# Optimization experiments

Hardware: AMD Instinct MI355X
Metric: run time of the kernel (lower is better)

## Reference

```python
import jax, jax.numpy as jnp
import numpy as np

N_NODES = 20000
N_EDGES = 320000
BERT_H = 768
GIN_H = 256
N_LAYERS = 3
EPS = 0.0  # gin_epsilon


def setup_inputs() -> dict:
    key = jax.random.key(0)
    ks = jax.random.split(key, 12)
    node_embed = jax.random.normal(ks[0], (N_NODES, BERT_H), dtype=jnp.float32)
    edge_weight = jax.random.uniform(ks[1], (N_EDGES,), dtype=jnp.float32)
    src = jax.random.randint(ks[2], (N_EDGES,), 0, N_NODES, dtype=jnp.int32)
    dst = jax.random.randint(ks[3], (N_EDGES,), 0, N_NODES, dtype=jnp.int32)
    s = 0.02
    W0 = jax.random.normal(ks[4], (BERT_H, GIN_H), dtype=jnp.float32) * s
    b0 = jnp.zeros((GIN_H,), dtype=jnp.float32)
    W1 = jax.random.normal(ks[5], (GIN_H, GIN_H), dtype=jnp.float32) * s
    b1 = jnp.zeros((GIN_H,), dtype=jnp.float32)
    W2 = jax.random.normal(ks[6], (GIN_H, GIN_H), dtype=jnp.float32) * s
    b2 = jnp.zeros((GIN_H,), dtype=jnp.float32)
    Wr = jax.random.normal(ks[7], (N_LAYERS * GIN_H, GIN_H), dtype=jnp.float32) * s
    br = jnp.zeros((GIN_H,), dtype=jnp.float32)
    return {"node_embed": node_embed, "edge_weight": edge_weight,
            "W0": W0, "b0": b0, "W1": W1, "b1": b1, "W2": W2, "b2": b2,
            "Wr": Wr, "br": br, "src": src, "dst": dst}


def _gin_layer(h, edge_weight, src, dst, W, b):
    # edge-weighted sum aggregation: agg_i = sum_{(j->i)} w_ji * h_j
    msgs = h[src] * edge_weight[:, None]          # [E, d]
    agg = jax.ops.segment_sum(msgs, dst, num_segments=N_NODES)  # [N, d]
    rst = (1.0 + EPS) * h + agg
    return jax.nn.relu(rst @ W + b)


def reference(node_embed, edge_weight, W0, b0, W1, b1, W2, b2, Wr, br, src, dst):
    params = [(W0, b0), (W1, b1), (W2, b2)]
    h = node_embed
    outs = []
    for (W, b) in params:
        h = _gin_layer(h, edge_weight, src, dst, W, b)
        outs.append(h)
    cat = jnp.concatenate(outs, axis=-1)          # [N, n_layers*gin_h]
    return jax.nn.relu(cat) @ Wr + br             # [N, gin_h]
```

## Files before the change

### kernel.cpp

```cpp
#include <hip/hip_runtime.h>

#define NN 20000
#define NE 320000
#define BH 768
#define GH 256

typedef __attribute__((ext_vector_type(8))) short short8;
typedef __attribute__((ext_vector_type(4))) float f32x4;

__device__ __forceinline__ ushort f2bf(float x) {
    union { float f; unsigned u; } v; v.f = x;
    unsigned r = (v.u + 0x7FFFu + ((v.u >> 16) & 1u)) >> 16;
    return (ushort)r;
}
__device__ __forceinline__ float bf2f(ushort h) {
    union { unsigned u; float f; } v; v.u = ((unsigned)h) << 16;
    return v.f;
}

__device__ __forceinline__ void gload_lds16(const void* g, void* l) {
    __builtin_amdgcn_global_load_lds(
        (const __attribute__((address_space(1))) void*)g,
        (__attribute__((address_space(3))) void*)l, 16, 0, 0);
}


__global__ void k_count(const int* __restrict__ dst, int* __restrict__ cnt, int E) {
    int i = blockIdx.x * blockDim.x + threadIdx.x;
    if (i < E) atomicAdd(&cnt[dst[i]], 1);
}

__global__ __launch_bounds__(1024)
void k_scan(const int* __restrict__ cnt, int* __restrict__ off,
            int* __restrict__ fill, int n) {
    __shared__ int sbuf[1024];
    const int tid  = threadIdx.x;
    const int base = tid * 20;
    int local[20];
    int s = 0;
    #pragma unroll
    for (int i = 0; i < 20; ++i) {
        const int idx = base + i;
        int v = (idx < n) ? cnt[idx] : 0;
        local[i] = s;
        s += v;
    }
    sbuf[tid] = s;
    __syncthreads();
    int sum = s;
    for (int ofs = 1; ofs < 1024; ofs <<= 1) {
        int other = (tid >= ofs) ? sbuf[tid - ofs] : 0;
        __syncthreads();
        sum += other;
        sbuf[tid] = sum;
        __syncthreads();
    }
    const int excl = sum - s;
    #pragma unroll
    for (int i = 0; i < 20; ++i) {
        const int idx = base + i;
        if (idx < n) { const int v = excl + local[i]; off[idx] = v; fill[idx] = v; }
    }
    if (tid == 1023) off[n] = sum;
}

__global__ void k_scatter(const int* __restrict__ src, const int* __restrict__ dst,
                          const float* __restrict__ w, int* __restrict__ fill,
                          int* __restrict__ csr_src, float* __restrict__ csr_w, int E) {
    int i = blockIdx.x * blockDim.x + threadIdx.x;
    if (i < E) {
        int d = dst[i];
        int p = atomicAdd(&fill[d], 1);
        csr_src[p] = src[i];
        csr_w[p]  = w[i];
    }
}


__global__ void k_split(const float* __restrict__ x, ushort* __restrict__ hi,
                        ushort* __restrict__ lo, int n4) {
    int i = blockIdx.x * blockDim.x + threadIdx.x;
    if (i >= n4) return;
    float4 v = ((const float4*)x)[i];
    ushort4 h, l;
    h.x = f2bf(v.x); l.x = f2bf(v.x - bf2f(h.x));
    h.y = f2bf(v.y); l.y = f2bf(v.y - bf2f(h.y));
    h.z = f2bf(v.z); l.z = f2bf(v.z - bf2f(h.z));
    h.w = f2bf(v.w); l.w = f2bf(v.w - bf2f(h.w));
    ((ushort4*)hi)[i] = h;
    ((ushort4*)lo)[i] = l;
}

__global__ void k_splitw(const float* __restrict__ W, ushort* __restrict__ hi,
                         ushort* __restrict__ lo, int K, int N) {
    int id = blockIdx.x * blockDim.x + threadIdx.x;
    if (id >= K * N) return;
    int n = id / K, k = id % K;
    float v = W[(size_t)k * N + n];
    ushort h = f2bf(v);
    hi[id] = h;
    lo[id] = f2bf(v - bf2f(h));
}


__global__ __launch_bounds__(256)
void k_gemm_mfma(const ushort* __restrict__ Ah, const ushort* __restrict__ Al,
                 int lda, int K,
                 const ushort* __restrict__ Bh, const ushort* __restrict__ Bl,
                 const float* __restrict__ bias,
                 float* __restrict__ C, int M) {
    __shared__ ushort As_h[64 * 32];
    __shared__ ushort As_l[64 * 32];
    __shared__ ushort Bs_h[128 * 32];
    __shared__ ushort Bs_l[128 * 32];

    const int t    = threadIdx.x;
    const int lane = t & 63;
    const int m0   = blockIdx.y * 64;
    const int n0   = blockIdx.x * 128;

    const int ra = t >> 2;
    const int sa = (t & 3) ^ ((ra >> 1) & 3);
    int rga = m0 + ra; if (rga > M - 1) rga = M - 1;
    const size_t aofs = (size_t)rga * lda + (size_t)(sa * 8);
    char* a_dst_h = (char*)As_h + ((t >> 6) << 10);
    char* a_dst_l = (char*)As_l + ((t >> 6) << 10);

    const int cb1 = t + 256;
    const int rb0 = t >> 2,   rb1 = cb1 >> 2;
    const int sb0 = (t & 3)   ^ ((rb0 >> 1) & 3);
    const int sb1 = (cb1 & 3) ^ ((rb1 >> 1) & 3);
    const size_t bofs0 = (size_t)(n0 + rb0) * K + (size_t)(sb0 * 8);
    const size_t bofs1 = (size_t)(n0 + rb1) * K + (size_t)(sb1 * 8);
    char* b_dst_h0 = (char*)Bs_h + ((t >> 6) << 10);
    char* b_dst_h1 = (char*)Bs_h + ((cb1 >> 6) << 10);
    char* b_dst_l0 = (char*)Bs_l + ((t >> 6) << 10);
    char* b_dst_l1 = (char*)Bs_l + ((cb1 >> 6) << 10);

    const int wm = (t >> 6) & 1;
    const int wn = t >> 7;

    f32x4 zero = (f32x4)0.0f;
    f32x4 acc[2][4];
    #pragma unroll
    for (int i = 0; i < 2; ++i)
        #pragma unroll
        for (int j = 0; j < 4; ++j) acc[i][j] = zero;

    const int fr  = lane & 15;
    const int fsl = lane >> 4;

    for (int k0 = 0; k0 < K; k0 += 32) {
        __syncthreads();
        gload_lds16(Ah + aofs + k0, a_dst_h);
        gload_lds16(Al + aofs + k0, a_dst_l);
        gload_lds16(Bh + bofs0 + k0, b_dst_h0);
        gload_lds16(Bh + bofs1 + k0, b_dst_h1);
        gload_lds16(Bl + bofs0 + k0, b_dst_l0);
        gload_lds16(Bl + bofs1 + k0, b_dst_l1);
        __syncthreads();

        short8 ah[2], al2[2], bh[4], bl[4];
        #pragma unroll
        for (int i = 0; i < 2; ++i) {
            const int r = wm * 32 + i * 16 + fr;
            const int s = fsl ^ ((r >> 1) & 3);
            ah[i]  = *(const short8*)(As_h + r * 32 + s * 8);
            al2[i] = *(const short8*)(As_l + r * 32 + s * 8);
        }
        #pragma unroll
        for (int j = 0; j < 4; ++j) {
            const int r = wn * 64 + j * 16 + fr;
            const int s = fsl ^ ((r >> 1) & 3);
            bh[j] = *(const short8*)(Bs_h + r * 32 + s * 8);
            bl[j] = *(const short8*)(Bs_l + r * 32 + s * 8);
        }
        #pragma unroll
        for (int i = 0; i < 2; ++i)
            #pragma unroll
            for (int j = 0; j < 4; ++j) {
                acc[i][j] = __builtin_amdgcn_mfma_f32_16x16x32_bf16(ah[i],  bh[j], acc[i][j], 0, 0, 0);
                acc[i][j] = __builtin_amdgcn_mfma_f32_16x16x32_bf16(ah[i],  bl[j], acc[i][j], 0, 0, 0);
                acc[i][j] = __builtin_amdgcn_mfma_f32_16x16x32_bf16(al2[i], bh[j], acc[i][j], 0, 0, 0);
            }
    }

    #pragma unroll
    for (int i = 0; i < 2; ++i) {
        #pragma unroll
        for (int j = 0; j < 4; ++j) {
            const int col = n0 + wn * 64 + j * 16 + fr;
            const int r0  = m0 + wm * 32 + i * 16 + ((lane >> 4) << 2);
            const float ba = bias ? bias[col] : 0.0f;
            #pragma unroll
            for (int q = 0; q < 4; ++q) {
                const int r = r0 + q;
                if (r < M) C[(size_t)r * 256 + col] = acc[i][j][q] + ba;
            }
        }
    }
}


__global__ __launch_bounds__(256)
void k_aggregate(const float* __restrict__ y,
                 const int* __restrict__ off,
                 const int* __restrict__ csr_src,
                 const float* __restrict__ csr_w,
                 const float* __restrict__ bias,
                 ushort* __restrict__ cat_h,
                 ushort* __restrict__ cat_l,
                 int n) {
    const int wave = blockIdx.x * (blockDim.x >> 6) + (threadIdx.x >> 6);
    const int lane = threadIdx.x & 63;
    if (wave >= n) return;
    const int c = lane * 4;

    float4 self = *(const float4*)(y + (size_t)wave * GH + c);
    float4 b    = *(const float4*)(bias + c);

    float4 a0 = make_float4(0.f, 0.f, 0.f, 0.f);
    float4 a1 = a0, a2 = a0, a3 = a0;
    const int e0 = off[wave], e1 = off[wave + 1];
    int e = e0;
    for (; e + 4 <= e1; e += 4) {
        const int   s0 = csr_src[e],     s1 = csr_src[e + 1];
        const int   s2 = csr_src[e + 2], s3 = csr_src[e + 3];
        const float w0 = csr_w[e],       w1 = csr_w[e + 1];
        const float w2 = csr_w[e + 2],   w3 = csr_w[e + 3];
        float4 v0 = *(const float4*)(y + (size_t)s0 * GH + c);
        float4 v1 = *(const float4*)(y + (size_t)s1 * GH + c);
        float4 v2 = *(const float4*)(y + (size_t)s2 * GH + c);
        float4 v3 = *(const float4*)(y + (size_t)s3 * GH + c);
        a0.x = fmaf(w0, v0.x, a0.x); a0.y = fmaf(w0, v0.y, a0.y);
        a0.z = fmaf(w0, v0.z, a0.z); a0.w = fmaf(w0, v0.w, a0.w);
        a1.x = fmaf(w1, v1.x, a1.x); a1.y = fmaf(w1, v1.y, a1.y);
        a1.z = fmaf(w1, v1.z, a1.z); a1.w = fmaf(w1, v1.w, a1.w);
        a2.x = fmaf(w2, v2.x, a2.x); a2.y = fmaf(w2, v2.y, a2.y);
        a2.z = fmaf(w2, v2.z, a2.z); a2.w = fmaf(w2, v2.w, a2.w);
        a3.x = fmaf(w3, v3.x, a3.x); a3.y = fmaf(w3, v3.y, a3.y);
        a3.z = fmaf(w3, v3.z, a3.z); a3.w = fmaf(w3, v3.w, a3.w);
    }
    for (; e < e1; ++e) {
        const int   s = csr_src[e];
        const float w = csr_w[e];
        float4 v = *(const float4*)(y + (size_t)s * GH + c);
        a0.x = fmaf(w, v.x, a0.x); a0.y = fmaf(w, v.y, a0.y);
        a0.z = fmaf(w, v.z, a0.z); a0.w = fmaf(w, v.w, a0.w);
    }
    float4 r;
    r.x = fmaxf(self.x + ((a0.x + a1.x) + (a2.x + a3.x)) + b.x, 0.f);
    r.y = fmaxf(self.y + ((a0.y + a1.y) + (a2.y + a3.y)) + b.y, 0.f);
    r.z = fmaxf(self.z + ((a0.z + a1.z) + (a2.z + a3.z)) + b.z, 0.f);
    r.w = fmaxf(self.w + ((a0.w + a1.w) + (a2.w + a3.w)) + b.w, 0.f);
    ushort4 h, l;
    h.x = f2bf(r.x); l.x = f2bf(r.x - bf2f(h.x));
    h.y = f2bf(r.y); l.y = f2bf(r.y - bf2f(h.y));
    h.z = f2bf(r.z); l.z = f2bf(r.z - bf2f(h.z));
    h.w = f2bf(r.w); l.w = f2bf(r.w - bf2f(h.w));
    *(ushort4*)(cat_h + (size_t)wave * BH + c) = h;
    *(ushort4*)(cat_l + (size_t)wave * BH + c) = l;
}


extern "C" void kernel_launch(void* const* d_in, const int* in_sizes, int n_in,
                              void* d_out, int out_size, void* d_ws, size_t ws_size,
                              hipStream_t stream) {
    const float* node_embed = (const float*)d_in[0];
    const float* edge_w     = (const float*)d_in[1];
    const float* W0 = (const float*)d_in[2];
    const float* b0 = (const float*)d_in[3];
    const float* W1 = (const float*)d_in[4];
    const float* b1 = (const float*)d_in[5];
    const float* W2 = (const float*)d_in[6];
    const float* b2 = (const float*)d_in[7];
    const float* Wr = (const float*)d_in[8];
    const float* br = (const float*)d_in[9];
    const int* src  = (const int*)d_in[10];
    const int* dst  = (const int*)d_in[11];
    float* out = (float*)d_out;

    char* p = (char*)d_ws;
    auto carve = [&](size_t bytes) {
        void* r = (void*)p;
        p += (bytes + 255) & ~(size_t)255;
        return r;
    };
    ushort* plane_h = (ushort*)carve((size_t)NN * BH * 2);
    ushort* plane_l = (ushort*)carve((size_t)NN * BH * 2);
    float*  y       = (float*) carve((size_t)NN * GH * 4);
    ushort* wt0_h = (ushort*)carve((size_t)GH * BH * 2);
    ushort* wt0_l = (ushort*)carve((size_t)GH * BH * 2);
    ushort* wt1_h = (ushort*)carve((size_t)GH * GH * 2);
    ushort* wt1_l = (ushort*)carve((size_t)GH * GH * 2);
    ushort* wt2_h = (ushort*)carve((size_t)GH * GH * 2);
    ushort* wt2_l = (ushort*)carve((size_t)GH * GH * 2);
    ushort* wtr_h = (ushort*)carve((size_t)GH * BH * 2);
    ushort* wtr_l = (ushort*)carve((size_t)GH * BH * 2);
    int*    cnt     = (int*)  carve((size_t)NN * 4);
    int*    off     = (int*)  carve((size_t)(NN + 1) * 4);
    int*    fill    = (int*)  carve((size_t)NN * 4);
    int*    csr_src = (int*)  carve((size_t)NE * 4);
    float*  csr_w   = (float*)carve((size_t)NE * 4);
    (void)ws_size; (void)n_in; (void)in_sizes; (void)out_size;

    hipMemsetAsync(cnt, 0, (size_t)NN * 4, stream);
    k_count<<<(NE + 255) / 256, 256, 0, stream>>>(dst, cnt, NE);
    k_scan<<<1, 1024, 0, stream>>>(cnt, off, fill, NN);
    k_scatter<<<(NE + 255) / 256, 256, 0, stream>>>(src, dst, edge_w, fill,
                                                    csr_src, csr_w, NE);

    const int n4 = NN * BH / 4;
    k_split<<<(n4 + 255) / 256, 256, 0, stream>>>(node_embed, plane_h, plane_l, n4);
    k_splitw<<<(BH * GH + 255) / 256, 256, 0, stream>>>(W0, wt0_h, wt0_l, BH, GH);
    k_splitw<<<(GH * GH + 255) / 256, 256, 0, stream>>>(W1, wt1_h, wt1_l, GH, GH);
    k_splitw<<<(GH * GH + 255) / 256, 256, 0, stream>>>(W2, wt2_h, wt2_l, GH, GH);
    k_splitw<<<(BH * GH + 255) / 256, 256, 0, stream>>>(Wr, wtr_h, wtr_l, BH, GH);

    dim3 gemm_grid(2, (NN + 63) / 64);
    const int agg_blocks = (NN + 3) / 4;

    k_gemm_mfma<<<gemm_grid, 256, 0, stream>>>(plane_h, plane_l, BH, BH,
                                               wt0_h, wt0_l, nullptr, y, NN);
    k_aggregate<<<agg_blocks, 256, 0, stream>>>(y, off, csr_src, csr_w, b0,
                                                plane_h + 0, plane_l + 0, NN);
    k_gemm_mfma<<<gemm_grid, 256, 0, stream>>>(plane_h, plane_l, BH, GH,
                                               wt1_h, wt1_l, nullptr, y, NN);
    k_aggregate<<<agg_blocks, 256, 0, stream>>>(y, off, csr_src, csr_w, b1,
                                                plane_h + GH, plane_l + GH, NN);
    k_gemm_mfma<<<gemm_grid, 256, 0, stream>>>(plane_h + GH, plane_l + GH, BH, GH,
                                               wt2_h, wt2_l, nullptr, y, NN);
    k_aggregate<<<agg_blocks, 256, 0, stream>>>(y, off, csr_src, csr_w, b2,
                                                plane_h + 2 * GH, plane_l + 2 * GH, NN);
    k_gemm_mfma<<<gemm_grid, 256, 0, stream>>>(plane_h, plane_l, BH, BH,
                                               wtr_h, wtr_l, br, out, NN);
}
```

Before: 457.4 us.

## Double-buffer LDS tiles in split-bf16 MFMA GEMM to overlap loads with compute

Turns the single LDS tile buffers of the bf16 hi/lo MFMA GEMM into two-stage ping-pong buffers. The loop now issues the global_load_lds for the next K-slice right after the barrier and then runs MFMAs on the current slice, dropping the second barrier per iteration. The goal is to hide global-to-LDS latency behind compute. The cost is doubled LDS use, which may lower occupancy, and overlap only happens if the compiler does not insert a full vmcnt wait before the LDS reads.

```diff
diff --git a/kernel.cpp b/kernel.cpp
--- a/kernel.cpp
+++ b/kernel.cpp
@@ -109,10 +109,10 @@
                  const ushort* __restrict__ Bh, const ushort* __restrict__ Bl,
                  const float* __restrict__ bias,
                  float* __restrict__ C, int M) {
-    __shared__ ushort As_h[64 * 32];
-    __shared__ ushort As_l[64 * 32];
-    __shared__ ushort Bs_h[128 * 32];
-    __shared__ ushort Bs_l[128 * 32];
+    __shared__ ushort As_h[2][64 * 32];
+    __shared__ ushort As_l[2][64 * 32];
+    __shared__ ushort Bs_h[2][128 * 32];
+    __shared__ ushort Bs_l[2][128 * 32];
 
     const int t    = threadIdx.x;
     const int lane = t & 63;
@@ -123,19 +123,14 @@
     const int sa = (t & 3) ^ ((ra >> 1) & 3);
     int rga = m0 + ra; if (rga > M - 1) rga = M - 1;
     const size_t aofs = (size_t)rga * lda + (size_t)(sa * 8);
-    char* a_dst_h = (char*)As_h + ((t >> 6) << 10);
-    char* a_dst_l = (char*)As_l + ((t >> 6) << 10);
-
     const int cb1 = t + 256;
     const int rb0 = t >> 2,   rb1 = cb1 >> 2;
     const int sb0 = (t & 3)   ^ ((rb0 >> 1) & 3);
     const int sb1 = (cb1 & 3) ^ ((rb1 >> 1) & 3);
     const size_t bofs0 = (size_t)(n0 + rb0) * K + (size_t)(sb0 * 8);
     const size_t bofs1 = (size_t)(n0 + rb1) * K + (size_t)(sb1 * 8);
-    char* b_dst_h0 = (char*)Bs_h + ((t >> 6) << 10);
-    char* b_dst_h1 = (char*)Bs_h + ((cb1 >> 6) << 10);
-    char* b_dst_l0 = (char*)Bs_l + ((t >> 6) << 10);
-    char* b_dst_l1 = (char*)Bs_l + ((cb1 >> 6) << 10);
+    const int d0 = (t >> 6) << 10;
+    const int d1 = (cb1 >> 6) << 10;
 
     const int wm = (t >> 6) & 1;
     const int wn = t >> 7;
@@ -150,30 +145,35 @@
     const int fr  = lane & 15;
     const int fsl = lane >> 4;
 
-    for (int k0 = 0; k0 < K; k0 += 32) {
+    auto STAGE = [&](int buf, int k0) {
+        gload_lds16(Ah + aofs + k0, (char*)As_h[buf] + d0);
+        gload_lds16(Al + aofs + k0, (char*)As_l[buf] + d0);
+        gload_lds16(Bh + bofs0 + k0, (char*)Bs_h[buf] + d0);
+        gload_lds16(Bh + bofs1 + k0, (char*)Bs_h[buf] + d1);
+        gload_lds16(Bl + bofs0 + k0, (char*)Bs_l[buf] + d0);
+        gload_lds16(Bl + bofs1 + k0, (char*)Bs_l[buf] + d1);
+    };
+
+    STAGE(0, 0);
+    int cur = 0;
+    for (int k0 = 0; k0 < K; k0 += 32, cur ^= 1) {
         __syncthreads();
-        gload_lds16(Ah + aofs + k0, a_dst_h);
-        gload_lds16(Al + aofs + k0, a_dst_l);
-        gload_lds16(Bh + bofs0 + k0, b_dst_h0);
-        gload_lds16(Bh + bofs1 + k0, b_dst_h1);
-        gload_lds16(Bl + bofs0 + k0, b_dst_l0);
-        gload_lds16(Bl + bofs1 + k0, b_dst_l1);
-        __syncthreads();
+        if (k0 + 32 < K) STAGE(cur ^ 1, k0 + 32);
 
         short8 ah[2], al2[2], bh[4], bl[4];
         #pragma unroll
         for (int i = 0; i < 2; ++i) {
             const int r = wm * 32 + i * 16 + fr;
             const int s = fsl ^ ((r >> 1) & 3);
-            ah[i]  = *(const short8*)(As_h + r * 32 + s * 8);
-            al2[i] = *(const short8*)(As_l + r * 32 + s * 8);
+            ah[i]  = *(const short8*)(&As_h[cur][0] + r * 32 + s * 8);
+            al2[i] = *(const short8*)(&As_l[cur][0] + r * 32 + s * 8);
         }
         #pragma unroll
         for (int j = 0; j < 4; ++j) {
             const int r = wn * 64 + j * 16 + fr;
             const int s = fsl ^ ((r >> 1) & 3);
-            bh[j] = *(const short8*)(Bs_h + r * 32 + s * 8);
-            bl[j] = *(const short8*)(Bs_l + r * 32 + s * 8);
+            bh[j] = *(const short8*)(&Bs_h[cur][0] + r * 32 + s * 8);
+            bl[j] = *(const short8*)(&Bs_l[cur][0] + r * 32 + s * 8);
         }
         #pragma unroll
         for (int i = 0; i < 2; ++i)
```

New measurement: 455.7 us. About the same (-0.4%).
